# Kernel optimization log

Hardware: AMD Instinct MI355X
Metric: run time of the kernel (lower is better)

Reference implementation:

```python
import jax, jax.numpy as jnp
import numpy as np

B, L, D, H = 4, 4096, 1024, 16
Dh = D // H
DECAY_INIT, DECAY_RANGE = 5.0, 1.0
LN_EPS = 1e-5


def setup_inputs() -> dict:
    key = jax.random.key(0)
    ks = jax.random.split(key, 5)
    s = 1.0 / np.sqrt(D)
    x = jax.random.normal(ks[0], (B, L, D), dtype=jnp.float32)
    Wq = jax.random.normal(ks[1], (D, D), dtype=jnp.float32) * s
    Wv = jax.random.normal(ks[2], (D, D), dtype=jnp.float32) * s
    Wo = jax.random.normal(ks[3], (D, D), dtype=jnp.float32) * s
    Wg = jax.random.normal(ks[4], (D, D), dtype=jnp.float32) * s
    # per-head decay logits, matching __init__: 5.0 + 1.0 * h / H
    beta = DECAY_INIT + DECAY_RANGE * (jnp.arange(H, dtype=jnp.float32) / H)
    ln_gamma = jnp.ones((D,), dtype=jnp.float32)
    ln_beta = jnp.zeros((D,), dtype=jnp.float32)
    return {"x": x, "Wq": Wq, "Wv": Wv, "Wo": Wo, "Wg": Wg,
            "beta": beta, "ln_gamma": ln_gamma, "ln_beta": ln_beta}


def _retention_scan(v, lam):
    # v: (B,L,H,Dh), lam: (H,); s_t = lam * s_{t-1} + v_t  (s_{-1} = 0)
    a = jnp.broadcast_to(lam[None, None, :, None], v.shape)

    def combine(c1, c2):
        a1, b1 = c1
        a2, b2 = c2
        return a1 * a2, a2 * b1 + b2

    _, s = jax.lax.associative_scan(combine, (a, v), axis=1)
    return s


def _layernorm(x, gamma, beta):
    mu = jnp.mean(x, axis=-1, keepdims=True)
    var = jnp.mean(jnp.square(x - mu), axis=-1, keepdims=True)
    return (x - mu) * jax.lax.rsqrt(var + LN_EPS) * gamma + beta


def reference(x, Wq, Wv, Wo, Wg, beta, ln_gamma, ln_beta):
    b, l, d = x.shape
    # decay lambda per head: (1 - 2^-beta) clamped to (tiny, 1 - 1e-9)
    tiny = jnp.finfo(jnp.float32).tiny
    lam = jnp.clip(1.0 - jnp.exp2(-beta), tiny, 1.0 - 1e-9)
    q = (x @ Wq.T).reshape(b, l, H, Dh)
    v = (x @ Wv.T).reshape(b, l, H, Dh)
    state = _retention_scan(v, lam)             # (B,L,H,Dh)
    ret = (q * state).reshape(b, l, d)          # per-timestep retention readout
    y = _layernorm(ret, ln_gamma, ln_beta)
    g = jax.nn.silu(x @ Wg.T)                   # swish gate
    out = (y * g) @ Wo.T
    return out
```

## Files before the change

### kernel.cpp

```cpp
#include <hip/hip_runtime.h>
#include <hip/hip_bf16.h>
#include <cfloat>

#define BB 4
#define LL 4096
#define DD 1024
#define HH 16
#define DHH 64
#define MM (BB * LL)
#define LN_EPS 1e-5f
#define LDQVG 3072
#define SCC 16
#define NCHUNK (LL / SCC)

typedef __hip_bfloat16 bf16;
typedef __attribute__((ext_vector_type(8))) short short8;
typedef __attribute__((ext_vector_type(4))) float f32x4;

struct bf16x4 { bf16 a, b, c, d; };
struct alignas(16) bf8 { bf16 e[8]; };

__device__ __forceinline__ float b2f(bf16 u) {
    union { unsigned int i; float f; } c;
    c.i = ((unsigned int)__bfloat16_as_ushort(u)) << 16;
    return c.f;
}

__device__ __forceinline__ float lam_of(const float* beta, int head) {
    float lam = 1.0f - exp2f(-beta[head]);
    return fminf(fmaxf(lam, 1.1754944e-38f), 1.0f - 1e-9f);
}

__global__ __launch_bounds__(256) void cvt_all(const float* __restrict__ x,
                                               const float* __restrict__ wq,
                                               const float* __restrict__ wv,
                                               const float* __restrict__ wg,
                                               const float* __restrict__ wo,
                                               bf16* __restrict__ xb,
                                               bf16* __restrict__ wb) {
    const int blk = blockIdx.x;
    const float* src;
    bf16* dst;
    size_t off;
    if (blk < 16384) {
        src = x; dst = xb; off = (size_t)blk * 1024;
    } else {
        int wblk  = blk - 16384;
        int which = wblk >> 10;
        src = (which == 0) ? wq : (which == 1) ? wv : (which == 2) ? wg : wo;
        dst = wb + (size_t)which * 1048576;
        off = (size_t)(wblk & 1023) * 1024;
    }
    size_t i = off + threadIdx.x * 4;
    float4 f = *(const float4*)(src + i);
    bf16x4 o;
    o.a = __float2bfloat16(f.x);
    o.b = __float2bfloat16(f.y);
    o.c = __float2bfloat16(f.z);
    o.d = __float2bfloat16(f.w);
    *(bf16x4*)(dst + i) = o;
}

__device__ __forceinline__ void async16(const bf16* g, bf16* l) {
    __builtin_amdgcn_global_load_lds(
        (const __attribute__((address_space(1))) void*)g,
        (__attribute__((address_space(3))) void*)l,
        16, 0, 0);
}

template <typename OutT, int KK>
__global__ __launch_bounds__(256, 2) void gemm_ring(const bf16* __restrict__ A,
                                                    const bf16* __restrict__ Bm,
                                                    OutT* __restrict__ C,
                                                    int ldc,
                                                    float* __restrict__ Sout,
                                                    const float* __restrict__ beta) {
    constexpr int BK    = 32;
    constexpr int NT    = KK / BK;
    constexpr int ASLOT = 256 * BK;
    constexpr int BSLOT = 128 * BK;

    __shared__ alignas(16) bf16 sA[3 * ASLOT];
    __shared__ alignas(16) bf16 sB[3 * BSLOT];

    const int t    = threadIdx.x;
    const int lane = t & 63;
    const int wave = t >> 6;
    const int wm   = wave >> 1;
    const int wn   = wave & 1;
    const int bm   = blockIdx.x;
    const int bn   = blockIdx.y;

    const int srow = t >> 2;
    const int cswz = ((t & 3) ^ ((srow >> 1) & 3)) * 8;
    const bf16* gA = A  + (size_t)(bm * 256 + srow) * KK + cswz;
    const bf16* gB = Bm + (size_t)(bn * 128 + srow) * KK + cswz;
    const size_t rstep = (size_t)64 * KK;
    bf16* const lA = sA + t * 8;
    bf16* const lB = sB + t * 8;

    const int f16  = lane & 15;
    const int swz8 = ((lane >> 4) ^ ((f16 >> 1) & 3)) * 8;
    const bf16* const rdA0 = sA + (wm * 128 + f16) * BK + swz8;
    const bf16* const rdB0 = sB + (wn * 64  + f16) * BK + swz8;

    f32x4 acc[8][4] = {};

    int slR = 0,         slR2 = 0;
    int slS = 2 * ASLOT, slS2 = 2 * BSLOT;

#pragma unroll
    for (int j = 0; j < 4; ++j) async16(gA + j * rstep, lA + j * 2048);
#pragma unroll
    for (int j = 0; j < 2; ++j) async16(gB + j * rstep, lB + j * 2048);
    gA += BK; gB += BK;
#pragma unroll
    for (int j = 0; j < 4; ++j) async16(gA + j * rstep, lA + ASLOT + j * 2048);
#pragma unroll
    for (int j = 0; j < 2; ++j) async16(gB + j * rstep, lB + BSLOT + j * 2048);
    gA += BK; gB += BK;
    asm volatile("s_waitcnt vmcnt(6)" ::: "memory");
    __builtin_amdgcn_s_barrier();

#define TILE(DOSTAGE, VMN)                                                     \
  {                                                                            \
    short8 a[8], b[4];                                                         \
    a[0] = *(const short8*)(rdA0 + slR);                                       \
    _Pragma("unroll") for (int ni = 0; ni < 4; ++ni)                           \
        b[ni] = *(const short8*)(rdB0 + ni * 512 + slR2);                      \
    _Pragma("unroll") for (int mi = 1; mi < 8; ++mi)                           \
        a[mi] = *(const short8*)(rdA0 + mi * 512 + slR);                       \
    if (DOSTAGE) {                                                             \
      _Pragma("unroll") for (int j = 0; j < 4; ++j)                            \
          async16(gA + j * rstep, lA + slS + j * 2048);                        \
      _Pragma("unroll") for (int j = 0; j < 2; ++j)                            \
          async16(gB + j * rstep, lB + slS2 + j * 2048);                       \
      gA += BK; gB += BK;                                                      \
    }                                                                          \
    __builtin_amdgcn_s_setprio(1);                                             \
    _Pragma("unroll") for (int mi = 0; mi < 8; ++mi)                           \
      _Pragma("unroll") for (int ni = 0; ni < 4; ++ni)                         \
        acc[mi][ni] = __builtin_amdgcn_mfma_f32_16x16x32_bf16(                 \
            a[mi], b[ni], acc[mi][ni], 0, 0, 0);                               \
    __builtin_amdgcn_s_setprio(0);                                             \
    if ((VMN) == 6)      asm volatile("s_waitcnt vmcnt(6)" ::: "memory");      \
    else if ((VMN) == 0) asm volatile("s_waitcnt vmcnt(0)" ::: "memory");      \
    if ((VMN) >= 0) __builtin_amdgcn_s_barrier();                              \
    slR  = (slR  == 2 * ASLOT) ? 0 : slR  + ASLOT;                             \
    slR2 = (slR2 == 2 * BSLOT) ? 0 : slR2 + BSLOT;                             \
    slS  = (slS  == 2 * ASLOT) ? 0 : slS  + ASLOT;                             \
    slS2 = (slS2 == 2 * BSLOT) ? 0 : slS2 + BSLOT;                             \
  }

#pragma unroll 1
    for (int T = 0; T < NT - 2; ++T) {
        TILE(true, 6);
    }
    TILE(false, 0);
    TILE(false, -1);

#undef TILE

    const int col0 = bn * 128 + wn * 64 + (lane & 15);
    const int row0 = bm * 256 + wm * 128 + ((lane >> 4) * 4);
#pragma unroll
    for (int mi = 0; mi < 8; ++mi) {
#pragma unroll
        for (int ni = 0; ni < 4; ++ni) {
#pragma unroll
            for (int r = 0; r < 4; ++r) {
                int row = row0 + mi * 16 + r;
                C[(size_t)row * ldc + col0 + ni * 16] = (OutT)acc[mi][ni][r];
            }
        }
    }

    if (Sout && bn >= 8 && bn < 16) {
        const int p0 = (lane >> 4) * 4;
        const int bglob = bm >> 4;
        const int c0 = ((bm & 15) * 16 + wm * 8);
#pragma unroll
        for (int ni = 0; ni < 4; ++ni) {
            const int f = col0 + ni * 16 - 1024;
            const float lam = lam_of(beta, f >> 6);
            const float l2g = __log2f(lam);
            float w[4];
#pragma unroll
            for (int r = 0; r < 4; ++r)
                w[r] = exp2f((float)(15 - p0 - r) * l2g);
#pragma unroll
            for (int mi = 0; mi < 8; ++mi) {
                float part = 0.0f;
#pragma unroll
                for (int r = 0; r < 4; ++r)
                    part = fmaf(w[r], acc[mi][ni][r], part);
                part += __shfl_xor(part, 16, 64);
                part += __shfl_xor(part, 32, 64);
                if (p0 == 0) {
                    const int cg = c0 + mi;
                    Sout[((size_t)bglob * NCHUNK + cg) * DD + f] = part;
                }
            }
        }
    }
}

__global__ __launch_bounds__(64) void scan_carry(const float* __restrict__ S,
                                                 float* __restrict__ T,
                                                 const float* __restrict__ beta) {
    const int gid = blockIdx.x * 64 + threadIdx.x;
    const int b = gid >> 10;
    const int f = gid & 1023;
    const float lam  = lam_of(beta, f >> 6);
    const float lamC = powf(lam, (float)SCC);

    const size_t base = (size_t)b * NCHUNK * DD + f;

    float v[16];
#pragma unroll
    for (int j = 0; j < 16; ++j) v[j] = S[base + (size_t)j * DD];

    float t = 0.0f;
    for (int c0 = 0; c0 < NCHUNK; c0 += 16) {
        float cur[16];
#pragma unroll
        for (int j = 0; j < 16; ++j) cur[j] = v[j];
        if (c0 + 16 < NCHUNK) {
#pragma unroll
            for (int j = 0; j < 16; ++j)
                v[j] = S[base + (size_t)(c0 + 16 + j) * DD];
        }
#pragma unroll
        for (int j = 0; j < 16; ++j) {
            T[base + (size_t)(c0 + j) * DD] = t;
            t = fmaf(t, lamC, cur[j]);
        }
    }
}

__global__ __launch_bounds__(128) void scan_apply_ln(const bf16* __restrict__ qvg,
                                                     const float* __restrict__ beta,
                                                     const float* __restrict__ T,
                                                     const float* __restrict__ gamma,
                                                     const float* __restrict__ betaln,
                                                     bf16* __restrict__ z) {
    __shared__ bf16 lds_ret[SCC][DD];

    const int c   = blockIdx.x;
    const int b   = blockIdx.y;
    const int tid = threadIdx.x;
    const int f0  = tid * 8;
    const float lam = lam_of(beta, f0 >> 6);

    const float* tp = T + ((size_t)(b * NCHUNK + c)) * DD + f0;
    float4 lo = *(const float4*)(tp);
    float4 hi = *(const float4*)(tp + 4);
    float s[8] = {lo.x, lo.y, lo.z, lo.w, hi.x, hi.y, hi.z, hi.w};

    const bf16* qp = qvg + ((size_t)(b * LL + c * SCC)) * LDQVG + f0;
    bf8 vv = *(const bf8*)(qp + 1024);
    bf8 qq = *(const bf8*)(qp);
#pragma unroll
    for (int t = 0; t < SCC; ++t) {
        bf8 vn, qn;
        if (t + 1 < SCC) {
            const size_t offn = (size_t)(t + 1) * LDQVG;
            vn = *(const bf8*)(qp + 1024 + offn);
            qn = *(const bf8*)(qp + offn);
        }
        bf8 o;
#pragma unroll
        for (int j = 0; j < 8; ++j) {
            s[j] = fmaf(s[j], lam, b2f(vv.e[j]));
            o.e[j] = __float2bfloat16(b2f(qq.e[j]) * s[j]);
        }
        *(bf8*)(&lds_ret[t][f0]) = o;
        if (t + 1 < SCC) { vv = vn; qq = qn; }
    }
    __syncthreads();

    const int lane = tid & 63;
    const int wv   = tid >> 6;

    bf8 gAp[8], gBp[8];
#pragma unroll
    for (int i = 0; i < 8; ++i) {
        const size_t row = (size_t)(b * LL + c * SCC + wv + 2 * i);
        const bf16* gp = qvg + row * LDQVG + 2048 + lane * 8;
        gAp[i] = *(const bf8*)(gp);
        gBp[i] = *(const bf8*)(gp + 512);
    }

    float gmA[8], btA[8], gmB[8], btB[8];
#pragma unroll
    for (int j = 0; j < 8; j += 4) {
        *(float4*)(gmA + j) = *(const float4*)(gamma  + lane * 8 + j);
        *(float4*)(btA + j) = *(const float4*)(betaln + lane * 8 + j);
        *(float4*)(gmB + j) = *(const float4*)(gamma  + 512 + lane * 8 + j);
        *(float4*)(btB + j) = *(const float4*)(betaln + 512 + lane * 8 + j);
    }

#pragma unroll
    for (int i = 0; i < 8; ++i) {
        const int t = wv + 2 * i;
        bf8 rA = *(const bf8*)(&lds_ret[t][lane * 8]);
        bf8 rB = *(const bf8*)(&lds_ret[t][512 + lane * 8]);

        float xa[8], xb2[8];
        float sum = 0.f, sq = 0.f;
#pragma unroll
        for (int j = 0; j < 8; ++j) {
            xa[j]  = b2f(rA.e[j]);
            xb2[j] = b2f(rB.e[j]);
            sum += xa[j] + xb2[j];
            sq  += xa[j] * xa[j] + xb2[j] * xb2[j];
        }
#pragma unroll
        for (int off = 32; off >= 1; off >>= 1) {
            sum += __shfl_xor(sum, off, 64);
            sq  += __shfl_xor(sq,  off, 64);
        }
        const float mu   = sum * (1.0f / DD);
        const float var  = sq * (1.0f / DD) - mu * mu;
        const float rstd = rsqrtf(var + LN_EPS);

        bf8 oA, oB;
#pragma unroll
        for (int j = 0; j < 8; ++j) {
            float ya = (xa[j]  - mu) * rstd * gmA[j] + btA[j];
            float yb = (xb2[j] - mu) * rstd * gmB[j] + btB[j];
            float ga = b2f(gAp[i].e[j]);
            float gb = b2f(gBp[i].e[j]);
            oA.e[j] = __float2bfloat16(ya * (ga / (1.0f + expf(-ga))));
            oB.e[j] = __float2bfloat16(yb * (gb / (1.0f + expf(-gb))));
        }
        const size_t row = (size_t)(b * LL + c * SCC + t);
        bf16* zp = z + row * DD + lane * 8;
        *(bf8*)(zp)       = oA;
        *(bf8*)(zp + 512) = oB;
    }
}

extern "C" void kernel_launch(void* const* d_in, const int* in_sizes, int n_in,
                              void* d_out, int out_size, void* d_ws, size_t ws_size,
                              hipStream_t stream) {
    const float* x     = (const float*)d_in[0];
    const float* Wq    = (const float*)d_in[1];
    const float* Wv    = (const float*)d_in[2];
    const float* Wo    = (const float*)d_in[3];
    const float* Wg    = (const float*)d_in[4];
    const float* beta  = (const float*)d_in[5];
    const float* ln_g  = (const float*)d_in[6];
    const float* ln_b  = (const float*)d_in[7];
    float* out = (float*)d_out;

    char* ws = (char*)d_ws;
    bf16*  xb   = (bf16*)ws;
    bf16*  wqb  = (bf16*)(ws + (size_t)32 * 1024 * 1024);
    float* Tbuf = (float*)(ws + (size_t)32 * 1024 * 1024);
    bf16*  wob  = wqb + 3 * 1048576;
    bf16*  qvg  = (bf16*)(ws + (size_t)40 * 1024 * 1024);
    bf16*  zb   = xb;
    float* Sbuf = out;

    cvt_all<<<dim3(16384 + 4096), dim3(256), 0, stream>>>(x, Wq, Wv, Wg, Wo, xb, wqb);

    gemm_ring<bf16, DD><<<dim3(MM / 256, LDQVG / 128), dim3(256), 0, stream>>>(
        xb, wqb, qvg, LDQVG, Sbuf, beta);

    scan_carry<<<dim3(64), dim3(64), 0, stream>>>(Sbuf, Tbuf, beta);
    scan_apply_ln<<<dim3(NCHUNK, BB), dim3(128), 0, stream>>>(
        qvg, beta, Tbuf, ln_g, ln_b, zb);

    gemm_ring<float, DD><<<dim3(MM / 256, DD / 128), dim3(256), 0, stream>>>(
        zb, wob, out, DD, nullptr, nullptr);
}
```

Before: 329.6 us.

## Split serial chunk-carry scan into three-level parallel scan; stagger GEMM block starts

The single-kernel carry scan, which ran only 64 blocks of 64 threads sequentially over 256 chunks, is replaced by three kernels. The first reduces each group of 16 chunks into a super-chunk sum, the second scans the 16 super-chunks, and the third expands the carries back to every chunk. This is meant to remove a long serial, low-occupancy phase, at the cost of two extra launches and an extra read of S. Separately, half of the GEMM blocks, chosen by a parity of their linear block index, sleep briefly after the prologue to stagger memory traffic.

```diff
diff --git a/kernel.cpp b/kernel.cpp
--- a/kernel.cpp
+++ b/kernel.cpp
@@ -12,6 +12,7 @@
 #define LDQVG 3072
 #define SCC 16
 #define NCHUNK (LL / SCC)
+#define NSUP 16
 
 typedef __hip_bfloat16 bf16;
 typedef __attribute__((ext_vector_type(8))) short short8;
@@ -121,6 +122,12 @@
     gA += BK; gB += BK;
     asm volatile("s_waitcnt vmcnt(6)" ::: "memory");
     __builtin_amdgcn_s_barrier();
+
+    {
+        const int lin  = blockIdx.x + (blockIdx.y << 6);
+        const int stag = (lin ^ (lin >> 8)) & 1;
+        if (stag) __builtin_amdgcn_s_sleep(21);
+    }
 
 #define TILE(DOSTAGE, VMN)                                                     \
   {                                                                            \
@@ -205,36 +212,68 @@
     }
 }
 
-__global__ __launch_bounds__(64) void scan_carry(const float* __restrict__ S,
-                                                 float* __restrict__ T,
-                                                 const float* __restrict__ beta) {
+__global__ __launch_bounds__(256) void carryA(const float* __restrict__ S,
+                                              float* __restrict__ W,
+                                              const float* __restrict__ beta) {
+    const int id = blockIdx.x * 256 + threadIdx.x;
+    const int f  = id & 1023;
+    const int s  = (id >> 10) & 15;
+    const int b  = id >> 14;
+    const float lam  = lam_of(beta, f >> 6);
+    const float lamC = powf(lam, (float)SCC);
+
+    const size_t base = (size_t)b * NCHUNK * DD + (size_t)(s * SCC) * DD + f;
+    float w = 0.0f;
+#pragma unroll
+    for (int j = 0; j < 16; ++j)
+        w = fmaf(w, lamC, S[base + (size_t)j * DD]);
+    W[((size_t)b * NSUP + s) * DD + f] = w;
+}
+
+__global__ __launch_bounds__(64) void carryB(const float* __restrict__ W,
+                                             float* __restrict__ TS,
+                                             const float* __restrict__ beta) {
     const int gid = blockIdx.x * 64 + threadIdx.x;
     const int b = gid >> 10;
     const int f = gid & 1023;
+    const float lam   = lam_of(beta, f >> 6);
+    const float lam16 = powf(lam, (float)(SCC * NSUP) / (float)NSUP);
+    const float lamS  = powf(lam16, (float)NSUP);
+
+    const size_t base = (size_t)b * NSUP * DD + f;
+    float w[NSUP];
+#pragma unroll
+    for (int s = 0; s < NSUP; ++s) w[s] = W[base + (size_t)s * DD];
+
+    float t = 0.0f;
+#pragma unroll
+    for (int s = 0; s < NSUP; ++s) {
+        TS[base + (size_t)s * DD] = t;
+        t = fmaf(t, lamS, w[s]);
+    }
+}
+
+__global__ __launch_bounds__(256) void carryC(const float* __restrict__ S,
+                                              const float* __restrict__ TS,
+                                              float* __restrict__ T,
+                                              const float* __restrict__ beta) {
+    const int id = blockIdx.x * 256 + threadIdx.x;
+    const int f  = id & 1023;
+    const int s  = (id >> 10) & 15;
+    const int b  = id >> 14;
     const float lam  = lam_of(beta, f >> 6);
     const float lamC = powf(lam, (float)SCC);
 
-    const size_t base = (size_t)b * NCHUNK * DD + f;
-
-    float v[16];
-#pragma unroll
-    for (int j = 0; j < 16; ++j) v[j] = S[base + (size_t)j * DD];
-
-    float t = 0.0f;
-    for (int c0 = 0; c0 < NCHUNK; c0 += 16) {
-        float cur[16];
-#pragma unroll
-        for (int j = 0; j < 16; ++j) cur[j] = v[j];
-        if (c0 + 16 < NCHUNK) {
-#pragma unroll
-            for (int j = 0; j < 16; ++j)
-                v[j] = S[base + (size_t)(c0 + 16 + j) * DD];
-        }
-#pragma unroll
-        for (int j = 0; j < 16; ++j) {
-            T[base + (size_t)(c0 + j) * DD] = t;
-            t = fmaf(t, lamC, cur[j]);
-        }
+    const size_t cbase = (size_t)b * NCHUNK * DD + (size_t)(s * SCC) * DD + f;
+    float sv[16];
+#pragma unroll
+    for (int j = 0; j < 16; ++j) sv[j] = S[cbase + (size_t)j * DD];
+
+    float t = TS[((size_t)b * NSUP + s) * DD + f];
+#pragma unroll
+    for (int j = 0; j < 16; ++j) {
+        T[cbase + (size_t)j * DD] = t;
+        t = fmaf(t, lamC, sv[j]);
     }
 }
 
@@ -355,20 +394,25 @@
     float* out = (float*)d_out;
 
     char* ws = (char*)d_ws;
-    bf16*  xb   = (bf16*)ws;
-    bf16*  wqb  = (bf16*)(ws + (size_t)32 * 1024 * 1024);
-    float* Tbuf = (float*)(ws + (size_t)32 * 1024 * 1024);
-    bf16*  wob  = wqb + 3 * 1048576;
-    bf16*  qvg  = (bf16*)(ws + (size_t)40 * 1024 * 1024);
-    bf16*  zb   = xb;
-    float* Sbuf = out;
+    bf16*  xb    = (bf16*)ws;
+    bf16*  wqb   = (bf16*)(ws + (size_t)32 * 1024 * 1024);
+    float* Tbuf  = (float*)(ws + (size_t)32 * 1024 * 1024);
+    float* Wsup  = (float*)(ws + (size_t)36 * 1024 * 1024);
+    float* TSsup = (float*)(ws + (size_t)36 * 1024 * 1024 + 262144);
+    bf16*  wob   = wqb + 3 * 1048576;
+    bf16*  qvg   = (bf16*)(ws + (size_t)40 * 1024 * 1024);
+    bf16*  zb    = xb;
+    float* Sbuf  = out;
 
     cvt_all<<<dim3(16384 + 4096), dim3(256), 0, stream>>>(x, Wq, Wv, Wg, Wo, xb, wqb);
 
     gemm_ring<bf16, DD><<<dim3(MM / 256, LDQVG / 128), dim3(256), 0, stream>>>(
         xb, wqb, qvg, LDQVG, Sbuf, beta);
 
-    scan_carry<<<dim3(64), dim3(64), 0, stream>>>(Sbuf, Tbuf, beta);
+    carryA<<<dim3(256), dim3(256), 0, stream>>>(Sbuf, Wsup, beta);
+    carryB<<<dim3(64),  dim3(64),  0, stream>>>(Wsup, TSsup, beta);
+    carryC<<<dim3(256), dim3(256), 0, stream>>>(Sbuf, TSsup, Tbuf, beta);
+
     scan_apply_ln<<<dim3(NCHUNK, BB), dim3(128), 0, stream>>>(
         qvg, beta, Tbuf, ln_g, ln_b, zb);
 
```

Measured after the change: 338.2 us. 1.03x slower.
